# Kernel optimization log

Measured on AMD Instinct MI355X. Metric: run time of the kernel, lower is better.

Reference implementation:

```python
import jax, jax.numpy as jnp
import numpy as np

B, S, I, H, O, L = 64, 1024, 128, 512, 128, 2

def _gru_layer(x, h0, Wzx, Wzh, bz, Wrx, Wrh, br, Wgx, Wgh, bg):
    # Precompute input projections for all timesteps: (B,S,H)
    xz = jnp.einsum('bsi,ih->bsh', x, Wzx)
    xr = jnp.einsum('bsi,ih->bsh', x, Wrx)
    xg = jnp.einsum('bsi,ih->bsh', x, Wgx)
    def step(h, inp):
        xz_t, xr_t, xg_t = inp
        z = jax.nn.sigmoid(xz_t + h @ Wzh + bz)
        r = jax.nn.sigmoid(xr_t + h @ Wrh + br)
        g = jnp.tanh(xg_t + (r * h) @ Wgh + bg)
        h_new = z * h + (1.0 - z) * g
        return h_new, h_new
    # scan over time: move S to leading axis
    xs = (jnp.swapaxes(xz, 0, 1), jnp.swapaxes(xr, 0, 1), jnp.swapaxes(xg, 0, 1))
    hT, ys = jax.lax.scan(step, h0, xs)
    return jnp.swapaxes(ys, 0, 1), hT  # (B,S,H), (B,H)

def setup_inputs() -> dict:
    key = jax.random.key(0)
    ks = jax.random.split(key, 32)
    d = {}
    d['input'] = jax.random.normal(ks[0], (B, S, I), dtype=jnp.float32)
    d['hidden_state'] = jnp.zeros((B, L, H), dtype=jnp.float32)
    kidx = 1
    for layer in range(L):
        din = I if layer == 0 else H
        sx = 1.0 / np.sqrt(din)
        sh = 1.0 / np.sqrt(H)
        for gate in ('z', 'r', 'g'):
            d[f'W{gate}x{layer}'] = jax.random.uniform(ks[kidx], (din, H), jnp.float32, -sx, sx); kidx += 1
            d[f'W{gate}h{layer}'] = jax.random.uniform(ks[kidx], (H, H), jnp.float32, -sh, sh); kidx += 1
            d[f'b{gate}{layer}'] = jax.random.uniform(ks[kidx], (H,), jnp.float32, -sh, sh); kidx += 1
    so = 1.0 / np.sqrt(H)
    d['Wout'] = jax.random.uniform(ks[kidx], (H, O), jnp.float32, -so, so); kidx += 1
    d['bout'] = jax.random.uniform(ks[kidx], (O,), jnp.float32, -so, so)
    return d

def reference(input, hidden_state,
              Wzx0, Wzh0, bz0, Wrx0, Wrh0, br0, Wgx0, Wgh0, bg0,
              Wzx1, Wzh1, bz1, Wrx1, Wrh1, br1, Wgx1, Wgh1, bg1,
              Wout, bout):
    params = [
        (Wzx0, Wzh0, bz0, Wrx0, Wrh0, br0, Wgx0, Wgh0, bg0),
        (Wzx1, Wzh1, bz1, Wrx1, Wrh1, br1, Wgx1, Wgh1, bg1),
    ]
    x = input
    finals = []
    for layer in range(L):
        h0 = hidden_state[:, layer, :]
        x, hT = _gru_layer(x, h0, *params[layer])
        finals.append(hT)
    layer_output = jnp.einsum('bsh,ho->bso', x, Wout) + bout  # (B,S,O)
    hidden_out = jnp.stack(finals, axis=1)  # (B,L,H)
    return layer_output, hidden_out
```

## Files before the change

kernel.cpp:

```cpp
#include <hip/hip_runtime.h>
#include <cstdint>
#include <cstddef>

#define BDIM 512
#define NWG  256

constexpr int B_ = 64, S_ = 1024, I_ = 128, H_ = 512, O_ = 128;
constexpr size_t HB = (size_t)H_ * B_;

constexpr size_t Y1_OFF  = 0;
constexpr size_t Y2_OFF  = Y1_OFF + 2 * HB;
constexpr size_t RH0_OFF = Y2_OFF + 2 * HB;
constexpr size_t RH1_OFF = RH0_OFF + HB;
constexpr size_t Z0_OFF  = RH1_OFF + HB;
constexpr size_t Z1_OFF  = Z0_OFF + HB;
constexpr size_t BAR_OFF = Z1_OFF + HB;
constexpr size_t BAR_WORDS = 34 * 64;
constexpr size_t SLAB_TOT = BAR_OFF + BAR_WORDS;
constexpr size_t XT_OFF  = SLAB_TOT;
constexpr size_t XT_FLOATS = (size_t)S_ * I_ * B_;
constexpr size_t WS_NEED_XT_BYTES = (XT_OFF + XT_FLOATS) * 4;

__device__ __forceinline__ float4 llc_load4(const float* p) {
  const unsigned long long* q = (const unsigned long long*)p;
  unsigned long long lo = __hip_atomic_load(q,     __ATOMIC_RELAXED, __HIP_MEMORY_SCOPE_AGENT);
  unsigned long long hi = __hip_atomic_load(q + 1, __ATOMIC_RELAXED, __HIP_MEMORY_SCOPE_AGENT);
  union { unsigned long long u[2]; float4 v; } c;
  c.u[0] = lo; c.u[1] = hi;
  return c.v;
}
__device__ __forceinline__ void llc_store4(float* p, float4 v) {
  union { float4 v; unsigned long long u[2]; } c; c.v = v;
  __hip_atomic_store((unsigned long long*)p,     c.u[0], __ATOMIC_RELAXED, __HIP_MEMORY_SCOPE_AGENT);
  __hip_atomic_store((unsigned long long*)p + 1, c.u[1], __ATOMIC_RELAXED, __HIP_MEMORY_SCOPE_AGENT);
}

__global__ void k_init(const float* __restrict__ hidden, float* __restrict__ ws) {
  int idx = blockIdx.x * 256 + threadIdx.x;
  if (idx < (int)(2 * HB)) {
    int l = idx >> 15, r = idx & 32767;
    int k = r >> 6, b = r & 63;
    ws[(l ? Y2_OFF : Y1_OFF) + HB + r] = hidden[b * 1024 + l * 512 + k];
  } else if (idx < (int)(2 * HB + BAR_WORDS)) {
    ((unsigned int*)(ws + BAR_OFF))[idx - 2 * HB] = 0u;
  }
}

__global__ void k_transpose_x(const float* __restrict__ in, float* __restrict__ Xt) {
  const size_t NQ = (size_t)B_ * S_ * I_ / 4;
  for (size_t q = (size_t)blockIdx.x * blockDim.x + threadIdx.x; q < NQ;
       q += (size_t)gridDim.x * blockDim.x) {
    int i4 = (int)(q & 31);
    int t  = (int)((q >> 5) & 1023);
    int b  = (int)(q >> 15);
    float4 v = *(const float4*)(in + ((size_t)b * 1024 + t) * 128 + i4 * 4);
    float* dst = Xt + (size_t)t * 8192 + (size_t)(i4 * 4) * 64 + b;
    dst[0] = v.x; dst[64] = v.y; dst[128] = v.z; dst[192] = v.w;
  }
}

__device__ __forceinline__ void fmas(float4& a, float s, const float4 h) {
  a.x = fmaf(s, h.x, a.x); a.y = fmaf(s, h.y, a.y);
  a.z = fmaf(s, h.z, a.z); a.w = fmaf(s, h.w, a.w);
}
__device__ __forceinline__ void fma16L(float4* acc, const float4* wA4, int k, float4 h) {
  #pragma unroll
  for (int g = 0; g < 4; ++g) {
    float4 w = wA4[g * 1024 + k];
    fmas(acc[g * 4 + 0], w.x, h); fmas(acc[g * 4 + 1], w.y, h);
    fmas(acc[g * 4 + 2], w.z, h); fmas(acc[g * 4 + 3], w.w, h);
  }
}
__device__ __forceinline__ void fma8L(float4* acc, const float4* wB4, int k, float4 h) {
  #pragma unroll
  for (int g = 0; g < 2; ++g) {
    float4 w = wB4[g * 1024 + k];
    fmas(acc[g * 4 + 0], w.x, h); fmas(acc[g * 4 + 1], w.y, h);
    fmas(acc[g * 4 + 2], w.z, h); fmas(acc[g * 4 + 3], w.w, h);
  }
}
__device__ __forceinline__ void red2(float4& v) {
  v.x += __shfl_xor(v.x, 8);  v.y += __shfl_xor(v.y, 8);
  v.z += __shfl_xor(v.z, 8);  v.w += __shfl_xor(v.w, 8);
  v.x += __shfl_xor(v.x, 16); v.y += __shfl_xor(v.y, 16);
  v.z += __shfl_xor(v.z, 16); v.w += __shfl_xor(v.w, 16);
}

__device__ __forceinline__ void grid_barrier(unsigned int* bar, unsigned int ph) {
  __syncthreads();
  asm volatile("" ::: "memory");
  if (threadIdx.x == 0) {
    const int g = (int)(blockIdx.x >> 4);
    unsigned int* grp_cnt  = bar + (size_t)g * 64;
    unsigned int* root_cnt = bar + 16 * 64;
    unsigned int* grp_gen  = bar + (size_t)(17 + g) * 64;
    unsigned int* root_gen = bar + 33 * 64;
    unsigned int r = __hip_atomic_fetch_add(grp_cnt, 1u, __ATOMIC_RELAXED, __HIP_MEMORY_SCOPE_AGENT);
    if (r == 16u * ph - 1u) {
      unsigned int rr = __hip_atomic_fetch_add(root_cnt, 1u, __ATOMIC_RELAXED, __HIP_MEMORY_SCOPE_AGENT);
      if (rr == 16u * ph - 1u) {
        __hip_atomic_store(root_gen, ph, __ATOMIC_RELAXED, __HIP_MEMORY_SCOPE_AGENT);
      } else {
        while (__hip_atomic_load(root_gen, __ATOMIC_RELAXED, __HIP_MEMORY_SCOPE_AGENT) < ph)
          __builtin_amdgcn_s_sleep(1);
      }
      __hip_atomic_store(grp_gen, ph, __ATOMIC_RELAXED, __HIP_MEMORY_SCOPE_AGENT);
    } else {
      while (__hip_atomic_load(grp_gen, __ATOMIC_RELAXED, __HIP_MEMORY_SCOPE_AGENT) < ph)
        __builtin_amdgcn_s_sleep(1);
    }
  }
  asm volatile("" ::: "memory");
  __syncthreads();
}

struct ScanArgs {
  float* ws;
  const float* xin;
  float* out;
  const float *Wzx0, *Wzh0, *bz0, *Wrx0, *Wrh0, *br0, *Wgx0, *Wgh0, *bg0;
  const float *Wzx1, *Wzh1, *bz1, *Wrx1, *Wrh1, *br1, *Wgx1, *Wgh1, *bg1;
  const float *Wout, *bout;
  int use_xt;
};

__launch_bounds__(BDIM, 1)
__global__ void k_scan(ScanArgs a) {
  float* ws = a.ws;
  unsigned int* bar = (unsigned int*)(ws + BAR_OFF);

  const int tid  = threadIdx.x;
  const int wg   = blockIdx.x;
  const int lane = tid & 63;
  const int wv   = tid >> 6;
  const int kt   = (wv << 3) | (lane >> 3);
  const int bq   = lane & 7;
  const int b4   = bq << 2;
  const int hi   = lane >> 5;

  const int  mA    = wg >> 6;
  const int  lA    = mA >> 1;
  const int  gA    = mA & 1;
  const int  cg    = (wg >> 1) & 31;
  const int  bg    = wg & 1;
  const int  jA0   = cg * 16;
  const int  b0    = bg * 32;
  const bool isL1A = (mA >= 2);
  const int  mB    = isL1A ? 0 : 1;
  const int  jB0   = (((mA & 1) << 5) | cg) * 8;
  const int  jO    = (((gA << 5) | cg)) * 2;

  __shared__ float4 wA4[4 * 1024];
  __shared__ float4 wB4[2 * 1024];
  __shared__ float2 wO2[512];
  __shared__ float4 pL[18 * 8 * 17];

  {
    const float* A0 = lA ? (gA ? a.Wrx1 : a.Wzx1) : (gA ? a.Wrh0 : a.Wzh0);
    const float* A1 = lA ? (gA ? a.Wrh1 : a.Wzh1) : (gA ? a.Wrx0 : a.Wzx0);
    const int KA1 = lA ? 512 : 128;
    for (int idx = tid; idx < 4096; idx += BDIM) {
      int c4 = idx >> 10, k = idx & 1023;
      int j = jA0 + c4 * 4;
      float4 w = make_float4(0.f, 0.f, 0.f, 0.f);
      if (k < 512)            w = *(const float4*)(A0 + (size_t)k * 512 + j);
      else if (k - 512 < KA1) w = *(const float4*)(A1 + (size_t)(k - 512) * 512 + j);
      wA4[idx] = w;
    }
    const float* B0 = mB ? a.Wgx1 : a.Wgh0;
    const float* B1 = mB ? a.Wgh1 : a.Wgx0;
    const int KB1 = mB ? 512 : 128;
    for (int idx = tid; idx < 2048; idx += BDIM) {
      int c4 = idx >> 10, k = idx & 1023;
      int j = jB0 + c4 * 4;
      float4 w = make_float4(0.f, 0.f, 0.f, 0.f);
      if (k < 512)            w = *(const float4*)(B0 + (size_t)k * 512 + j);
      else if (k - 512 < KB1) w = *(const float4*)(B1 + (size_t)(k - 512) * 512 + j);
      wB4[idx] = w;
    }
    if (isL1A)
      for (int idx = tid; idx < 512; idx += BDIM)
        wO2[idx] = *(const float2*)(a.Wout + (size_t)idx * 128 + jO);
  }
  const float* bAv = lA ? (gA ? a.br1 : a.bz1) : (gA ? a.br0 : a.bz0);
  float biasA = 0.f, biasB = 0.f, boutc = 0.f;
  if (tid < 128)                biasA = bAv[jA0 + (tid >> 3)];
  else if (tid < 144 && isL1A)  boutc = a.bout[jO + ((tid >> 3) & 1)];
  if (tid < 64)                 biasB = (mB ? a.bg1 : a.bg0)[jB0 + (tid >> 3)];
  __syncthreads();

  const float* XT = ws + XT_OFF;
  unsigned int ph = 1;

  for (int tau = 0; tau <= S_ + 1; ++tau) {
    const bool doL0 = (tau < S_);
    const bool doL1 = (tau >= 1) && (tau <= S_);
    const int slotP = (tau + 1) & 1;
    const int slotQ = tau & 1;
    const float* y1p = ws + Y1_OFF + (size_t)slotP * HB;
    const float* y2p = ws + Y2_OFF + (size_t)slotQ * HB;
    float* y1w = ws + Y1_OFF + (size_t)slotQ * HB;
    float* y2w = ws + Y2_OFF + (size_t)slotP * HB;

    const bool actL = isL1A ? doL1 : doL0;
    const bool outW = isL1A && (tau >= 2);
    float4 acc[16];
    #pragma unroll
    for (int c = 0; c < 16; ++c) acc[c] = make_float4(0.f, 0.f, 0.f, 0.f);
    float4 accO0 = make_float4(0.f, 0.f, 0.f, 0.f);
    float4 accO1 = make_float4(0.f, 0.f, 0.f, 0.f);

    if (actL) {
      if (!isL1A) {
        if (a.use_xt) {
          const float* XTt = XT + (size_t)tau * 8192;
          #pragma unroll
          for (int i = 0; i < 2; ++i) {
            const int k = i * 64 + kt;
            float4 h = *(const float4*)(XTt + (size_t)k * 64 + b0 + b4);
            fma16L(acc, wA4, 512 + k, h);
          }
        } else {
          #pragma unroll
          for (int i = 0; i < 2; ++i) {
            const int k = i * 64 + kt;
            float4 h;
            h.x = a.xin[(size_t)(b0 + b4 + 0) * 131072 + (size_t)tau * 128 + k];
            h.y = a.xin[(size_t)(b0 + b4 + 1) * 131072 + (size_t)tau * 128 + k];
            h.z = a.xin[(size_t)(b0 + b4 + 2) * 131072 + (size_t)tau * 128 + k];
            h.w = a.xin[(size_t)(b0 + b4 + 3) * 131072 + (size_t)tau * 128 + k];
            fma16L(acc, wA4, 512 + k, h);
          }
        }
      }
      #pragma unroll 4
      for (int i = 0; i < 8; ++i) {
        const int k = i * 64 + kt;
        float4 h = llc_load4(y1p + (size_t)k * 64 + b0 + b4);
        fma16L(acc, wA4, k, h);
      }
    }
    if (isL1A && (actL || outW)) {
      #pragma unroll 4
      for (int i = 0; i < 8; ++i) {
        const int k = i * 64 + kt;
        float4 h = llc_load4(y2p + (size_t)k * 64 + b0 + b4);
        fma16L(acc, wA4, 512 + k, h);
        float2 wo = wO2[k];
        fmas(accO0, wo.x, h); fmas(accO1, wo.y, h);
      }
    }
    if (actL) {
      #pragma unroll
      for (int c = 0; c < 16; ++c) red2(acc[c]);
      if ((lane & 24) == 0) {
        #pragma unroll
        for (int c = 0; c < 16; ++c) pL[(c * 8 + bq) * 17 + (wv << 1) + hi] = acc[c];
      }
    }
    if (outW) {
      red2(accO0); red2(accO1);
      if ((lane & 24) == 0) {
        pL[(16 * 8 + bq) * 17 + (wv << 1) + hi] = accO0;
        pL[(17 * 8 + bq) * 17 + (wv << 1) + hi] = accO1;
      }
    }
    __syncthreads();
    if (tid < 128) {
      if (actL) {
        const int c = tid >> 3, bqc = tid & 7;
        const float4* row = &pL[(c * 8 + bqc) * 17];
        float4 s = make_float4(biasA, biasA, biasA, biasA);
        #pragma unroll
        for (int w = 0; w < 16; ++w) {
          float4 p = row[w];
          s.x += p.x; s.y += p.y; s.z += p.z; s.w += p.w;
        }
        float4 v;
        v.x = 1.0f / (1.0f + __expf(-s.x)); v.y = 1.0f / (1.0f + __expf(-s.y));
        v.z = 1.0f / (1.0f + __expf(-s.z)); v.w = 1.0f / (1.0f + __expf(-s.w));
        const size_t jb = (size_t)(jA0 + c) * 64 + b0 + bqc * 4;
        if (gA == 0) {
          llc_store4(ws + (lA ? Z1_OFF : Z0_OFF) + jb, v);
        } else {
          float4 hp = llc_load4((lA ? y2p : y1p) + jb);
          v.x *= hp.x; v.y *= hp.y; v.z *= hp.z; v.w *= hp.w;
          llc_store4(ws + (lA ? RH1_OFF : RH0_OFF) + jb, v);
        }
      }
    } else if (tid < 144 && outW) {
      const int oc = (tid >> 3) & 1, bqc = tid & 7;
      const float4* row = &pL[((16 + oc) * 8 + bqc) * 17];
      float4 s = make_float4(boutc, boutc, boutc, boutc);
      #pragma unroll
      for (int w = 0; w < 16; ++w) {
        float4 p = row[w];
        s.x += p.x; s.y += p.y; s.z += p.z; s.w += p.w;
      }
      const int bb = b0 + bqc * 4;
      const size_t ob = ((size_t)bb * 1024 + (tau - 2)) * 128 + jO + oc;
      a.out[ob]          = s.x;
      a.out[ob + 131072] = s.y;
      a.out[ob + 262144] = s.z;
      a.out[ob + 393216] = s.w;
    }

    grid_barrier(bar, ph++);

    const bool actB = mB ? doL1 : doL0;
    float4 accB[8];
    #pragma unroll
    for (int c = 0; c < 8; ++c) accB[c] = make_float4(0.f, 0.f, 0.f, 0.f);
    if (actB) {
      if (!mB) {
        if (a.use_xt) {
          const float* XTt = XT + (size_t)tau * 8192;
          #pragma unroll
          for (int i = 0; i < 2; ++i) {
            const int k = i * 64 + kt;
            float4 h = *(const float4*)(XTt + (size_t)k * 64 + b0 + b4);
            fma8L(accB, wB4, 512 + k, h);
          }
        } else {
          #pragma unroll
          for (int i = 0; i < 2; ++i) {
            const int k = i * 64 + kt;
            float4 h;
            h.x = a.xin[(size_t)(b0 + b4 + 0) * 131072 + (size_t)tau * 128 + k];
            h.y = a.xin[(size_t)(b0 + b4 + 1) * 131072 + (size_t)tau * 128 + k];
            h.z = a.xin[(size_t)(b0 + b4 + 2) * 131072 + (size_t)tau * 128 + k];
            h.w = a.xin[(size_t)(b0 + b4 + 3) * 131072 + (size_t)tau * 128 + k];
            fma8L(accB, wB4, 512 + k, h);
          }
        }
        #pragma unroll 4
        for (int i = 0; i < 8; ++i) {
          const int k = i * 64 + kt;
          float4 h = llc_load4(ws + RH0_OFF + (size_t)k * 64 + b0 + b4);
          fma8L(accB, wB4, k, h);
        }
      } else {
        #pragma unroll 4
        for (int i = 0; i < 8; ++i) {
          const int k = i * 64 + kt;
          float4 h = llc_load4(y1p + (size_t)k * 64 + b0 + b4);
          fma8L(accB, wB4, k, h);
        }
        #pragma unroll 4
        for (int i = 0; i < 8; ++i) {
          const int k = i * 64 + kt;
          float4 h = llc_load4(ws + RH1_OFF + (size_t)k * 64 + b0 + b4);
          fma8L(accB, wB4, 512 + k, h);
        }
      }
      #pragma unroll
      for (int c = 0; c < 8; ++c) red2(accB[c]);
      if ((lane & 24) == 0) {
        #pragma unroll
        for (int c = 0; c < 8; ++c) pL[(c * 8 + bq) * 17 + (wv << 1) + hi] = accB[c];
      }
    }
    __syncthreads();
    if (actB && tid < 64) {
      const int c = tid >> 3, bqc = tid & 7;
      const float4* row = &pL[(c * 8 + bqc) * 17];
      float4 s = make_float4(biasB, biasB, biasB, biasB);
      #pragma unroll
      for (int w = 0; w < 16; ++w) {
        float4 p = row[w];
        s.x += p.x; s.y += p.y; s.z += p.z; s.w += p.w;
      }
      float4 g;
      g.x = tanhf(s.x); g.y = tanhf(s.y); g.z = tanhf(s.z); g.w = tanhf(s.w);
      const size_t jb = (size_t)(jB0 + c) * 64 + b0 + bqc * 4;
      float4 z  = llc_load4(ws + (mB ? Z1_OFF : Z0_OFF) + jb);
      float4 hp = llc_load4((mB ? y2p : y1p) + jb);
      float4 hn;
      hn.x = fmaf(z.x, hp.x - g.x, g.x);
      hn.y = fmaf(z.y, hp.y - g.y, g.y);
      hn.z = fmaf(z.z, hp.z - g.z, g.z);
      hn.w = fmaf(z.w, hp.w - g.w, g.w);
      llc_store4((mB ? y2w : y1w) + jb, hn);
    }

    grid_barrier(bar, ph++);
  }
}

__global__ void k_hidden(const float* __restrict__ ws, float* __restrict__ out) {
  int idx = blockIdx.x * 256 + threadIdx.x;
  int b = idx >> 10, rem = idx & 1023, l = rem >> 9, j = rem & 511;
  const float* src = ws + (l ? Y2_OFF : Y1_OFF) + HB + (size_t)j * 64 + b;
  out[(size_t)B_ * S_ * O_ + idx] = *src;
}

extern "C" void kernel_launch(void* const* d_in, const int* in_sizes, int n_in,
                              void* d_out, int out_size, void* d_ws, size_t ws_size,
                              hipStream_t stream) {
  const float* input  = (const float*)d_in[0];
  const float* hidden = (const float*)d_in[1];
  const float* Wzx0 = (const float*)d_in[2],  *Wzh0 = (const float*)d_in[3],  *bz0 = (const float*)d_in[4];
  const float* Wrx0 = (const float*)d_in[5],  *Wrh0 = (const float*)d_in[6],  *br0 = (const float*)d_in[7];
  const float* Wgx0 = (const float*)d_in[8],  *Wgh0 = (const float*)d_in[9],  *bg0 = (const float*)d_in[10];
  const float* Wzx1 = (const float*)d_in[11], *Wzh1 = (const float*)d_in[12], *bz1 = (const float*)d_in[13];
  const float* Wrx1 = (const float*)d_in[14], *Wrh1 = (const float*)d_in[15], *br1 = (const float*)d_in[16];
  const float* Wgx1 = (const float*)d_in[17], *Wgh1 = (const float*)d_in[18], *bg1 = (const float*)d_in[19];
  const float* Wout = (const float*)d_in[20], *bout = (const float*)d_in[21];
  float* ws = (float*)d_ws;
  float* out = (float*)d_out;

  const int use_xt = (ws_size >= WS_NEED_XT_BYTES) ? 1 : 0;

  k_init<<<265, 256, 0, stream>>>(hidden, ws);
  if (use_xt) k_transpose_x<<<2048, 256, 0, stream>>>(input, ws + XT_OFF);

  ScanArgs sa{ws, input, out,
              Wzx0, Wzh0, bz0, Wrx0, Wrh0, br0, Wgx0, Wgh0, bg0,
              Wzx1, Wzh1, bz1, Wrx1, Wrh1, br1, Wgx1, Wgh1, bg1,
              Wout, bout, use_xt};
  k_scan<<<dim3(NWG), dim3(BDIM), 0, stream>>>(sa);

  k_hidden<<<256, 256, 0, stream>>>(ws, out);
}
```

Measured before the change: 16.77 ms.

## Split grid barrier into arrive/wait and skew layer pipeline to overlap independent work

After: 18.05 ms. 7.6% more time.

```diff
diff --git a/kernel.cpp b/kernel.cpp
--- a/kernel.cpp
+++ b/kernel.cpp
@@ -9,7 +9,7 @@
 constexpr size_t HB = (size_t)H_ * B_;
 
 constexpr size_t Y1_OFF  = 0;
-constexpr size_t Y2_OFF  = Y1_OFF + 2 * HB;
+constexpr size_t Y2_OFF  = Y1_OFF + 4 * HB;
 constexpr size_t RH0_OFF = Y2_OFF + 2 * HB;
 constexpr size_t RH1_OFF = RH0_OFF + HB;
 constexpr size_t Z0_OFF  = RH1_OFF + HB;
@@ -40,7 +40,8 @@
   if (idx < (int)(2 * HB)) {
     int l = idx >> 15, r = idx & 32767;
     int k = r >> 6, b = r & 63;
-    ws[(l ? Y2_OFF : Y1_OFF) + HB + r] = hidden[b * 1024 + l * 512 + k];
+    size_t dst = l ? (Y2_OFF + HB) : (Y1_OFF + 3 * HB);
+    ws[dst + r] = hidden[b * 1024 + l * 512 + k];
   } else if (idx < (int)(2 * HB + BAR_WORDS)) {
     ((unsigned int*)(ws + BAR_OFF))[idx - 2 * HB] = 0u;
   }
@@ -86,29 +87,27 @@
   v.z += __shfl_xor(v.z, 16); v.w += __shfl_xor(v.w, 16);
 }
 
-__device__ __forceinline__ void grid_barrier(unsigned int* bar, unsigned int ph) {
+__device__ __forceinline__ void bar_arrive(unsigned int* bar, unsigned int ph) {
   __syncthreads();
   asm volatile("" ::: "memory");
   if (threadIdx.x == 0) {
     const int g = (int)(blockIdx.x >> 4);
-    unsigned int* grp_cnt  = bar + (size_t)g * 64;
-    unsigned int* root_cnt = bar + 16 * 64;
-    unsigned int* grp_gen  = bar + (size_t)(17 + g) * 64;
-    unsigned int* root_gen = bar + 33 * 64;
-    unsigned int r = __hip_atomic_fetch_add(grp_cnt, 1u, __ATOMIC_RELAXED, __HIP_MEMORY_SCOPE_AGENT);
+    unsigned int r = __hip_atomic_fetch_add(bar + (size_t)g * 64, 1u,
+                                            __ATOMIC_RELAXED, __HIP_MEMORY_SCOPE_AGENT);
     if (r == 16u * ph - 1u) {
-      unsigned int rr = __hip_atomic_fetch_add(root_cnt, 1u, __ATOMIC_RELAXED, __HIP_MEMORY_SCOPE_AGENT);
-      if (rr == 16u * ph - 1u) {
-        __hip_atomic_store(root_gen, ph, __ATOMIC_RELAXED, __HIP_MEMORY_SCOPE_AGENT);
-      } else {
-        while (__hip_atomic_load(root_gen, __ATOMIC_RELAXED, __HIP_MEMORY_SCOPE_AGENT) < ph)
-          __builtin_amdgcn_s_sleep(1);
-      }
-      __hip_atomic_store(grp_gen, ph, __ATOMIC_RELAXED, __HIP_MEMORY_SCOPE_AGENT);
-    } else {
-      while (__hip_atomic_load(grp_gen, __ATOMIC_RELAXED, __HIP_MEMORY_SCOPE_AGENT) < ph)
-        __builtin_amdgcn_s_sleep(1);
-    }
+      unsigned int rr = __hip_atomic_fetch_add(bar + 16 * 64, 1u,
+                                               __ATOMIC_RELAXED, __HIP_MEMORY_SCOPE_AGENT);
+      if (rr == 16u * ph - 1u)
+        __hip_atomic_store(bar + 33 * 64, ph, __ATOMIC_RELAXED, __HIP_MEMORY_SCOPE_AGENT);
+    }
+  }
+  asm volatile("" ::: "memory");
+}
+__device__ __forceinline__ void bar_wait(unsigned int* bar, unsigned int ph) {
+  asm volatile("" ::: "memory");
+  if (threadIdx.x == 0) {
+    while (__hip_atomic_load(bar + 33 * 64, __ATOMIC_RELAXED, __HIP_MEMORY_SCOPE_AGENT) < ph)
+      __builtin_amdgcn_s_sleep(1);
   }
   asm volatile("" ::: "memory");
   __syncthreads();
@@ -190,20 +189,19 @@
   __syncthreads();
 
   const float* XT = ws + XT_OFF;
-  unsigned int ph = 1;
-
-  for (int tau = 0; tau <= S_ + 1; ++tau) {
+
+  for (int tau = 0; tau <= S_ + 2; ++tau) {
     const bool doL0 = (tau < S_);
-    const bool doL1 = (tau >= 1) && (tau <= S_);
-    const int slotP = (tau + 1) & 1;
-    const int slotQ = tau & 1;
-    const float* y1p = ws + Y1_OFF + (size_t)slotP * HB;
-    const float* y2p = ws + Y2_OFF + (size_t)slotQ * HB;
-    float* y1w = ws + Y1_OFF + (size_t)slotQ * HB;
-    float* y2w = ws + Y2_OFF + (size_t)slotP * HB;
+    const bool doL1 = (tau >= 2) && (tau <= S_ + 1);
+    const float* y1p = ws + Y1_OFF + (size_t)((tau + 3) & 3) * HB;
+    const float* y1x = ws + Y1_OFF + (size_t)((tau + 2) & 3) * HB;
+    const float* y2p = ws + Y2_OFF + (size_t)((tau + 1) & 1) * HB;
+    float* y1w = ws + Y1_OFF + (size_t)(tau & 3) * HB;
+    float* y2w = ws + Y2_OFF + (size_t)(tau & 1) * HB;
 
     const bool actL = isL1A ? doL1 : doL0;
-    const bool outW = isL1A && (tau >= 2);
+    const bool outW = isL1A && (tau >= 3);
+
     float4 acc[16];
     #pragma unroll
     for (int c = 0; c < 16; ++c) acc[c] = make_float4(0.f, 0.f, 0.f, 0.f);
@@ -211,7 +209,14 @@
     float4 accO1 = make_float4(0.f, 0.f, 0.f, 0.f);
 
     if (actL) {
-      if (!isL1A) {
+      if (isL1A) {
+        #pragma unroll
+        for (int i = 0; i < 8; ++i) {
+          const int k = i * 64 + kt;
+          float4 h = llc_load4(y1x + (size_t)k * 64 + b0 + b4);
+          fma16L(acc, wA4, k, h);
+        }
+      } else {
         if (a.use_xt) {
           const float* XTt = XT + (size_t)tau * 8192;
           #pragma unroll
@@ -233,7 +238,11 @@
           }
         }
       }
-      #pragma unroll 4
+    }
+    if (tau) bar_wait(bar, 2u * tau);
+
+    if (actL && !isL1A) {
+      #pragma unroll
       for (int i = 0; i < 8; ++i) {
         const int k = i * 64 + kt;
         float4 h = llc_load4(y1p + (size_t)k * 64 + b0 + b4);
@@ -241,7 +250,7 @@
       }
     }
     if (isL1A && (actL || outW)) {
-      #pragma unroll 4
+      #pragma unroll
       for (int i = 0; i < 8; ++i) {
         const int k = i * 64 + kt;
         float4 h = llc_load4(y2p + (size_t)k * 64 + b0 + b4);
@@ -298,21 +307,28 @@
         s.x += p.x; s.y += p.y; s.z += p.z; s.w += p.w;
       }
       const int bb = b0 + bqc * 4;
-      const size_t ob = ((size_t)bb * 1024 + (tau - 2)) * 128 + jO + oc;
+      const size_t ob = ((size_t)bb * 1024 + (tau - 3)) * 128 + jO + oc;
       a.out[ob]          = s.x;
       a.out[ob + 131072] = s.y;
       a.out[ob + 262144] = s.z;
       a.out[ob + 393216] = s.w;
     }
 
-    grid_barrier(bar, ph++);
+    bar_arrive(bar, 2u * tau + 1u);
 
     const bool actB = mB ? doL1 : doL0;
     float4 accB[8];
     #pragma unroll
     for (int c = 0; c < 8; ++c) accB[c] = make_float4(0.f, 0.f, 0.f, 0.f);
     if (actB) {
-      if (!mB) {
+      if (mB) {
+        #pragma unroll
+        for (int i = 0; i < 8; ++i) {
+          const int k = i * 64 + kt;
+          float4 h = llc_load4(y1x + (size_t)k * 64 + b0 + b4);
+          fma8L(accB, wB4, k, h);
+        }
+      } else {
         if (a.use_xt) {
           const float* XTt = XT + (size_t)tau * 8192;
           #pragma unroll
@@ -333,25 +349,18 @@
             fma8L(accB, wB4, 512 + k, h);
           }
         }
-        #pragma unroll 4
-        for (int i = 0; i < 8; ++i) {
-          const int k = i * 64 + kt;
-          float4 h = llc_load4(ws + RH0_OFF + (size_t)k * 64 + b0 + b4);
-          fma8L(accB, wB4, k, h);
-        }
-      } else {
-        #pragma unroll 4
-        for (int i = 0; i < 8; ++i) {
-          const int k = i * 64 + kt;
-          float4 h = llc_load4(y1p + (size_t)k * 64 + b0 + b4);
-          fma8L(accB, wB4, k, h);
-        }
-        #pragma unroll 4
-        for (int i = 0; i < 8; ++i) {
-          const int k = i * 64 + kt;
-          float4 h = llc_load4(ws + RH1_OFF + (size_t)k * 64 + b0 + b4);
-          fma8L(accB, wB4, 512 + k, h);
-        }
+      }
+    }
+    bar_wait(bar, 2u * tau + 1u);
+
+    if (actB) {
+      const float* rhs = mB ? (ws + RH1_OFF) : (ws + RH0_OFF);
+      const int koff = mB ? 512 : 0;
+      #pragma unroll
+      for (int i = 0; i < 8; ++i) {
+        const int k = i * 64 + kt;
+        float4 h = llc_load4(rhs + (size_t)k * 64 + b0 + b4);
+        fma8L(accB, wB4, koff + k, h);
       }
       #pragma unroll
       for (int c = 0; c < 8; ++c) red2(accB[c]);
@@ -383,14 +392,14 @@
       llc_store4((mB ? y2w : y1w) + jb, hn);
     }
 
-    grid_barrier(bar, ph++);
+    bar_arrive(bar, 2u * tau + 2u);
   }
 }
 
 __global__ void k_hidden(const float* __restrict__ ws, float* __restrict__ out) {
   int idx = blockIdx.x * 256 + threadIdx.x;
   int b = idx >> 10, rem = idx & 1023, l = rem >> 9, j = rem & 511;
-  const float* src = ws + (l ? Y2_OFF : Y1_OFF) + HB + (size_t)j * 64 + b;
+  const float* src = ws + (l ? (Y2_OFF + HB) : (Y1_OFF + 3 * HB)) + (size_t)j * 64 + b;
   out[(size_t)B_ * S_ * O_ + idx] = *src;
 }
 
```
